# Kernel tuning notes

Measured on AMD Instinct MI355X. Metric: run time of the kernel, lower is better.

Reference implementation:

```python
import jax, jax.numpy as jnp
import numpy as np

K_BITS = 4
V_BITS = 4
GROUP_SIZE = 64
EPS = 1e-8


def _quant_dequant_per_token(x, bits):
    # TurboQuantProd: symmetric per-token (per head_dim vector) absmax quantization.
    qmax = 2.0 ** (bits - 1) - 1.0
    scale = jnp.maximum(jnp.max(jnp.abs(x), axis=-1, keepdims=True) / qmax, EPS)
    return jnp.clip(jnp.round(x / scale), -qmax, qmax) * scale


def _quant_dequant_grouped(x, bits, group_size):
    # TurboQuantValue: symmetric grouped absmax quantization along head_dim.
    shp = x.shape
    xg = x.reshape(shp[:-1] + (shp[-1] // group_size, group_size))
    qmax = 2.0 ** (bits - 1) - 1.0
    scale = jnp.maximum(jnp.max(jnp.abs(xg), axis=-1, keepdims=True) / qmax, EPS)
    dq = jnp.clip(jnp.round(xg / scale), -qmax, qmax) * scale
    return dq.reshape(shp)


def setup_inputs() -> dict:
    key = jax.random.key(0)
    kq, kk, kv = jax.random.split(key, 3)
    B, H, S, D = 2, 16, 2048, 128
    query = jax.random.normal(kq, (B, H, S, D), dtype=jnp.float32)
    k = jax.random.normal(kk, (B, H, S, D), dtype=jnp.float32)
    v = jax.random.normal(kv, (B, H, S, D), dtype=jnp.float32)
    causal_mask = jnp.tril(jnp.ones((S, S), dtype=bool))[None, None]  # [1,1,S,S]
    return {"query": query, "key": k, "value": v, "causal_mask": causal_mask}


def reference(query, key, value, causal_mask):
    # Non-protected path: quantize K per-token, V grouped, then fused dequant + SDPA.
    head_dim = query.shape[-1]
    scale = 1.0 / np.sqrt(head_dim).astype(np.float32)
    dq_key = _quant_dequant_per_token(key, K_BITS)
    dq_value = _quant_dequant_grouped(value, V_BITS, GROUP_SIZE)
    scores = jnp.einsum('bhqd,bhkd->bhqk', query, dq_key) * scale
    scores = jnp.where(causal_mask, scores, -jnp.inf)
    weights = jax.nn.softmax(scores, axis=-1)
    output = jnp.einsum('bhqk,bhkd->bhqd', weights, dq_value)
    return (output, weights)
```

## Files before the change

### kernel.cpp

```cpp
#include <hip/hip_runtime.h>

#define SQ 2048
#define DD 128
#define BHN 32
#define SC2 0.12751741934f

typedef __attribute__((ext_vector_type(8))) short bf16x8;
typedef __attribute__((ext_vector_type(4))) float f32x4;

__device__ __forceinline__ unsigned short f2bf(float x){
  unsigned int u = __float_as_uint(x);
  unsigned int r = (u + 0x7FFFu + ((u >> 16) & 1u)) >> 16;
  return (unsigned short)r;
}
__device__ __forceinline__ unsigned pack2bf(float a, float b){
  return (unsigned)f2bf(a) | ((unsigned)f2bf(b) << 16);
}

__device__ __forceinline__ void gl_lds16(const void* g, void* l){
  __builtin_amdgcn_global_load_lds(
      (const __attribute__((address_space(1))) unsigned int*)g,
      (__attribute__((address_space(3))) unsigned int*)l, 16, 0, 0);
}

__device__ __forceinline__ void nt_store4(float* p, f32x4 v){
  __builtin_nontemporal_store(v, (f32x4*)p);
}

__global__ __launch_bounds__(256) void qd_kernel(const float* __restrict__ K,
                                                 const float* __restrict__ V,
                                                 char* __restrict__ dqK,
                                                 char* __restrict__ dqVt){
  __shared__ float Vlds[128*65];
  const int t = threadIdx.x;
  const int bh = blockIdx.x >> 5;
  const int stile = blockIdx.x & 31;
  const int tt = t >> 2;
  const int q4 = t & 3;
  const int s = stile*64 + tt;
  const long ebase = ((long)(bh*SQ + s))*DD + 32*q4;

  float vals[32];
  {
    const float4* kp = (const float4*)(K + ebase);
    float am = 0.f;
    #pragma unroll
    for (int j=0;j<8;j++){
      float4 v4 = kp[j];
      vals[4*j+0]=v4.x; vals[4*j+1]=v4.y; vals[4*j+2]=v4.z; vals[4*j+3]=v4.w;
      am = fmaxf(am, fmaxf(fmaxf(fabsf(v4.x),fabsf(v4.y)),fmaxf(fabsf(v4.z),fabsf(v4.w))));
    }
    am = fmaxf(am, __shfl_xor(am,1));
    am = fmaxf(am, __shfl_xor(am,2));
    const float sc = fmaxf(am/7.0f, 1e-8f);
    #pragma unroll
    for (int j=0;j<32;j++){
      float qv = rintf(vals[j]/sc);
      qv = fminf(7.f, fmaxf(-7.f, qv));
      vals[j] = qv*sc;
    }
    const long rowb = ((long)(bh*SQ + s))*256;
    const int swz = (s & 7) << 4;
    #pragma unroll
    for (int c=0;c<4;c++){
      uint4 w;
      w.x = pack2bf(vals[8*c+0], vals[8*c+1]);
      w.y = pack2bf(vals[8*c+2], vals[8*c+3]);
      w.z = pack2bf(vals[8*c+4], vals[8*c+5]);
      w.w = pack2bf(vals[8*c+6], vals[8*c+7]);
      *(uint4*)(dqK + rowb + ((64*q4 + 16*c) ^ swz)) = w;
    }
  }
  {
    const float4* vp = (const float4*)(V + ebase);
    float am = 0.f;
    #pragma unroll
    for (int j=0;j<8;j++){
      float4 v4 = vp[j];
      vals[4*j+0]=v4.x; vals[4*j+1]=v4.y; vals[4*j+2]=v4.z; vals[4*j+3]=v4.w;
      am = fmaxf(am, fmaxf(fmaxf(fabsf(v4.x),fabsf(v4.y)),fmaxf(fabsf(v4.z),fabsf(v4.w))));
    }
    am = fmaxf(am, __shfl_xor(am,1));
    const float sc = fmaxf(am/7.0f, 1e-8f);
    #pragma unroll
    for (int j=0;j<32;j++){
      float qv = rintf(vals[j]/sc);
      qv = fminf(7.f, fmaxf(-7.f, qv));
      Vlds[(32*q4 + j)*65 + tt] = qv*sc;
    }
  }
  __syncthreads();
  #pragma unroll
  for (int m=0;m<4;m++){
    const int chunk = m*256 + t;
    const int d = chunk >> 3;
    const int c = chunk & 7;
    uint4 w;
    const float* f = &Vlds[d*65 + 8*c];
    w.x = pack2bf(f[0], f[1]);
    w.y = pack2bf(f[2], f[3]);
    w.z = pack2bf(f[4], f[5]);
    w.w = pack2bf(f[6], f[7]);
    const long ob = ((long)(bh*DD + d))*4096 + (long)stile*128 + ((16*c) ^ ((d&7)<<4));
    *(uint4*)(dqVt + ob) = w;
  }
}

__global__ __launch_bounds__(256,2) void attn_fused(const float* __restrict__ Q,
    const char* __restrict__ dqK, const char* __restrict__ dqVt,
    float* __restrict__ Out, float* __restrict__ Wout){
  __shared__ __attribute__((aligned(16))) char Kt[2][16384];
  __shared__ __attribute__((aligned(16))) char Vt[2][16384];
  __shared__ __attribute__((aligned(16))) char Et[4][4096];

  const int bid = blockIdx.x;
  const int xcd = bid & 7;
  const int loc = bid >> 3;
  const int bh  = xcd*4 + (loc & 3);
  const int p   = loc >> 2;
  const int t = threadIdx.x;
  const int lane = t & 63;
  const int w = t >> 6;
  const int s = w >> 1;
  const int ws = w & 1;
  const int l15 = lane & 15, l4 = lane >> 4;
  const int swz = (l15 & 7) << 4;

  const int qt   = s ? p : (31 - p);
  const int q0   = qt * 64;
  const int nktA = 32 - p;
  const int myNkt = qt + 1;
  const int rbase = q0 + 32*ws;

  bf16x8 qa[2][4];
  #pragma unroll
  for (int g=0; g<2; ++g){
    const float* qb = Q + ((long)(bh*SQ) + rbase + 16*g + l15)*DD + 8*l4;
    #pragma unroll
    for (int kk=0;kk<4;kk++){
      float4 a = *(const float4*)(qb + 32*kk);
      float4 b = *(const float4*)(qb + 32*kk + 4);
      bf16x8 r;
      r[0]=(short)f2bf(a.x); r[1]=(short)f2bf(a.y); r[2]=(short)f2bf(a.z); r[3]=(short)f2bf(a.w);
      r[4]=(short)f2bf(b.x); r[5]=(short)f2bf(b.y); r[6]=(short)f2bf(b.z); r[7]=(short)f2bf(b.w);
      qa[g][kk]=r;
    }
  }

  const char* Kb = dqK + (long)bh*SQ*256;
  const char* Vb = dqVt + (long)bh*DD*4096;

  const f32x4 z4 = {0.f,0.f,0.f,0.f};
  f32x4 oacc[2][8] = {{z4,z4,z4,z4,z4,z4,z4,z4},{z4,z4,z4,z4,z4,z4,z4,z4}};
  float ssum[2] = {0.f, 0.f};
  char* eb = &Et[w][0];

  auto stageKV = [&](int buf, int kt){
    const char* ks = Kb + (long)kt*16384;
    #pragma unroll
    for (int i=0;i<4;i++)
      gl_lds16(ks + i*4096 + t*16, &Kt[buf][i*4096 + t*16]);
    const char* vs = Vb + (long)kt*128;
    #pragma unroll
    for (int i=0;i<4;i++)
      gl_lds16(vs + (long)(i*32 + (t>>3))*4096 + (t&7)*16, &Vt[buf][i*4096 + t*16]);
  };

  stageKV(0, 0);
  __syncthreads();
  int cur = 0;
  for (int kt=0; kt<nktA; ++kt){
    if (kt+1 < nktA) stageKV(cur^1, kt+1);

    if (kt < myNkt){
      f32x4 sacc[2][4] = {{z4,z4,z4,z4},{z4,z4,z4,z4}};
      {
        const char* kbase = &Kt[cur][0] + l15*256;
        __builtin_amdgcn_s_setprio(1);
        #pragma unroll
        for (int cf=0;cf<4;cf++){
          #pragma unroll
          for (int kk=0;kk<4;kk++){
            bf16x8 kb = *(const bf16x8*)(kbase + cf*4096 + ((64*kk+16*l4) ^ swz));
            sacc[0][cf] = __builtin_amdgcn_mfma_f32_16x16x32_bf16(kb, qa[0][kk], sacc[0][cf], 0,0,0);
            sacc[1][cf] = __builtin_amdgcn_mfma_f32_16x16x32_bf16(kb, qa[1][kk], sacc[1][cf], 0,0,0);
          }
        }
        __builtin_amdgcn_s_setprio(0);
      }

      const int k0 = kt*64;
      if (kt < qt){
        #pragma unroll
        for (int g=0; g<2; ++g){
          const int lr = 16*g + l15;
          #pragma unroll
          for (int cf=0;cf<4;cf++){
            float e0 = exp2f(sacc[g][cf][0]*SC2);
            float e1 = exp2f(sacc[g][cf][1]*SC2);
            float e2 = exp2f(sacc[g][cf][2]*SC2);
            float e3 = exp2f(sacc[g][cf][3]*SC2);
            ssum[g] += (e0+e1) + (e2+e3);
            uint2 wp; wp.x = pack2bf(e0,e1); wp.y = pack2bf(e2,e3);
            *(uint2*)(eb + lr*128 + ((32*cf + 8*l4) ^ swz)) = wp;
          }
        }
      } else {
        #pragma unroll
        for (int g=0; g<2; ++g){
          const int lr = 16*g + l15;
          const int qrow = rbase + lr;
          #pragma unroll
          for (int cf=0;cf<4;cf++){
            const int tok0 = k0 + 16*cf + 4*l4;
            float e0 = (tok0+0 <= qrow) ? exp2f(sacc[g][cf][0]*SC2) : 0.f;
            float e1 = (tok0+1 <= qrow) ? exp2f(sacc[g][cf][1]*SC2) : 0.f;
            float e2 = (tok0+2 <= qrow) ? exp2f(sacc[g][cf][2]*SC2) : 0.f;
            float e3 = (tok0+3 <= qrow) ? exp2f(sacc[g][cf][3]*SC2) : 0.f;
            ssum[g] += (e0+e1) + (e2+e3);
            uint2 wp; wp.x = pack2bf(e0,e1); wp.y = pack2bf(e2,e3);
            *(uint2*)(eb + lr*128 + ((32*cf + 8*l4) ^ swz)) = wp;
          }
        }
      }

      {
        const char* vbase = &Vt[cur][0] + l15*128;
        __builtin_amdgcn_s_setprio(1);
        #pragma unroll
        for (int kc=0;kc<2;kc++){
          const int eo = (64*kc + 16*l4) ^ swz;
          bf16x8 ea0 = *(const bf16x8*)(eb + l15*128 + eo);
          bf16x8 ea1 = *(const bf16x8*)(eb + (16+l15)*128 + eo);
          #pragma unroll
          for (int df=0;df<8;df++){
            bf16x8 vv = *(const bf16x8*)(vbase + df*2048 + eo);
            oacc[0][df] = __builtin_amdgcn_mfma_f32_16x16x32_bf16(ea0, vv, oacc[0][df], 0,0,0);
            oacc[1][df] = __builtin_amdgcn_mfma_f32_16x16x32_bf16(ea1, vv, oacc[1][df], 0,0,0);
          }
        }
        __builtin_amdgcn_s_setprio(0);
      }
    }
    __syncthreads();
    cur ^= 1;
  }

  float si[2];
  #pragma unroll
  for (int g=0; g<2; ++g){
    float sm = ssum[g];
    sm += __shfl_xor(sm, 16);
    sm += __shfl_xor(sm, 32);
    si[g] = 1.0f / sm;
    float invr[4];
    #pragma unroll
    for (int i=0;i<4;i++) invr[i] = __shfl(si[g], 4*l4+i);
    float* ob = Out + ((long)(bh*SQ) + rbase + 16*g)*DD;
    #pragma unroll
    for (int df=0;df<8;df++){
      #pragma unroll
      for (int i=0;i<4;i++)
        ob[(4*l4+i)*DD + 16*df + l15] = oacc[g][df][i]*invr[i];
    }
  }

  float* Wbase = Wout + (long)bh*SQ*SQ;
  float* wrow0 = Wbase + (long)(rbase + l15)*SQ;
  float* wrow1 = Wbase + (long)(rbase + 16 + l15)*SQ;

  for (int kt=0; kt<myNkt; ++kt){
    const int k0 = kt*64;
    const char* kr = Kb + (long)kt*16384 + l15*256;

    bf16x8 kb[4][4];
    #pragma unroll
    for (int cf=0;cf<4;cf++){
      #pragma unroll
      for (int kk=0;kk<4;kk++)
        kb[cf][kk] = *(const bf16x8*)(kr + cf*4096 + ((64*kk+16*l4) ^ swz));
    }

    f32x4 sacc[2][4] = {{z4,z4,z4,z4},{z4,z4,z4,z4}};
    __builtin_amdgcn_s_setprio(1);
    #pragma unroll
    for (int cf=0;cf<4;cf++){
      #pragma unroll
      for (int kk=0;kk<4;kk++){
        sacc[0][cf] = __builtin_amdgcn_mfma_f32_16x16x32_bf16(kb[cf][kk], qa[0][kk], sacc[0][cf], 0,0,0);
        sacc[1][cf] = __builtin_amdgcn_mfma_f32_16x16x32_bf16(kb[cf][kk], qa[1][kk], sacc[1][cf], 0,0,0);
      }
    }
    __builtin_amdgcn_s_setprio(0);

    if (kt < qt){
      #pragma unroll
      for (int cf=0;cf<4;cf++){
        const int tok0 = k0 + 16*cf + 4*l4;
        f32x4 wv;
        wv[0] = exp2f(sacc[0][cf][0]*SC2)*si[0];
        wv[1] = exp2f(sacc[0][cf][1]*SC2)*si[0];
        wv[2] = exp2f(sacc[0][cf][2]*SC2)*si[0];
        wv[3] = exp2f(sacc[0][cf][3]*SC2)*si[0];
        nt_store4(wrow0 + tok0, wv);
        wv[0] = exp2f(sacc[1][cf][0]*SC2)*si[1];
        wv[1] = exp2f(sacc[1][cf][1]*SC2)*si[1];
        wv[2] = exp2f(sacc[1][cf][2]*SC2)*si[1];
        wv[3] = exp2f(sacc[1][cf][3]*SC2)*si[1];
        nt_store4(wrow1 + tok0, wv);
      }
    } else {
      const int qrow0 = rbase + l15;
      const int qrow1 = rbase + 16 + l15;
      #pragma unroll
      for (int cf=0;cf<4;cf++){
        const int tok0 = k0 + 16*cf + 4*l4;
        f32x4 wv;
        wv[0] = (tok0+0 <= qrow0) ? exp2f(sacc[0][cf][0]*SC2)*si[0] : 0.f;
        wv[1] = (tok0+1 <= qrow0) ? exp2f(sacc[0][cf][1]*SC2)*si[0] : 0.f;
        wv[2] = (tok0+2 <= qrow0) ? exp2f(sacc[0][cf][2]*SC2)*si[0] : 0.f;
        wv[3] = (tok0+3 <= qrow0) ? exp2f(sacc[0][cf][3]*SC2)*si[0] : 0.f;
        nt_store4(wrow0 + tok0, wv);
        wv[0] = (tok0+0 <= qrow1) ? exp2f(sacc[1][cf][0]*SC2)*si[1] : 0.f;
        wv[1] = (tok0+1 <= qrow1) ? exp2f(sacc[1][cf][1]*SC2)*si[1] : 0.f;
        wv[2] = (tok0+2 <= qrow1) ? exp2f(sacc[1][cf][2]*SC2)*si[1] : 0.f;
        wv[3] = (tok0+3 <= qrow1) ? exp2f(sacc[1][cf][3]*SC2)*si[1] : 0.f;
        nt_store4(wrow1 + tok0, wv);
      }
    }
  }

  const int z0 = myNkt*64;
  if (z0 < SQ){
    const f32x4 zz = {0.f,0.f,0.f,0.f};
    for (int rr=0;rr<32;rr++){
      float* row = Wbase + (long)(rbase + rr)*SQ;
      for (int c = z0 + 4*lane; c < SQ; c += 256)
        nt_store4(row + c, zz);
    }
  }
}

extern "C" void kernel_launch(void* const* d_in, const int* in_sizes, int n_in,
                              void* d_out, int out_size, void* d_ws, size_t ws_size,
                              hipStream_t stream) {
  const float* Q = (const float*)d_in[0];
  const float* K = (const float*)d_in[1];
  const float* V = (const float*)d_in[2];
  float* Out = (float*)d_out;
  float* Wout = (float*)d_out + (size_t)BHN*SQ*DD;
  char* dqK  = (char*)d_ws;
  char* dqVt = (char*)d_ws + (size_t)BHN*SQ*DD*2;

  qd_kernel<<<BHN*32, 256, 0, stream>>>(K, V, dqK, dqVt);
  attn_fused<<<512, 256, 0, stream>>>(Q, dqK, dqVt, Out, Wout);
}
```

Measured before the change: 261.9 us.

## Pair long and short query tiles per wave and use plain stores for weights

Each wave now owns 16 rows of a long tile (qtA = 31-p) and 16 rows of a short tile (qtB = p), instead of splitting waves into long and short halves. Every wave therefore does about the same work, and the B half of the MFMA work is skipped once it passes its causal limit. Block ordering also changes so that p interleaves small and large values. The weight and zero-fill stores switch from nontemporal to ordinary stores. The aim is to remove intra-block wave imbalance, since short-tile waves used to sit idle at barriers; the cost is extra branching inside the loops.

```diff
diff --git a/kernel.cpp b/kernel.cpp
--- a/kernel.cpp
+++ b/kernel.cpp
@@ -21,10 +21,6 @@
   __builtin_amdgcn_global_load_lds(
       (const __attribute__((address_space(1))) unsigned int*)g,
       (__attribute__((address_space(3))) unsigned int*)l, 16, 0, 0);
-}
-
-__device__ __forceinline__ void nt_store4(float* p, f32x4 v){
-  __builtin_nontemporal_store(v, (f32x4*)p);
 }
 
 __global__ __launch_bounds__(256) void qd_kernel(const float* __restrict__ K,
@@ -117,25 +113,26 @@
   const int xcd = bid & 7;
   const int loc = bid >> 3;
   const int bh  = xcd*4 + (loc & 3);
-  const int p   = loc >> 2;
+  const int i   = loc >> 2;
+  const int p   = (i < 8) ? i : (23 - i);
   const int t = threadIdx.x;
   const int lane = t & 63;
   const int w = t >> 6;
-  const int s = w >> 1;
-  const int ws = w & 1;
   const int l15 = lane & 15, l4 = lane >> 4;
   const int swz = (l15 & 7) << 4;
 
-  const int qt   = s ? p : (31 - p);
-  const int q0   = qt * 64;
-  const int nktA = 32 - p;
-  const int myNkt = qt + 1;
-  const int rbase = q0 + 32*ws;
+  const int qtA = 31 - p, qtB = p;
+  const int q0A = qtA*64, q0B = qtB*64;
+  const int nktA = qtA + 1;
+  const int nktB = qtB + 1;
+  const int rA = q0A + 16*w + l15;
+  const int rB = q0B + 16*w + l15;
 
   bf16x8 qa[2][4];
   #pragma unroll
   for (int g=0; g<2; ++g){
-    const float* qb = Q + ((long)(bh*SQ) + rbase + 16*g + l15)*DD + 8*l4;
+    const int qrow = g ? rB : rA;
+    const float* qb = Q + ((long)(bh*SQ) + qrow)*DD + 8*l4;
     #pragma unroll
     for (int kk=0;kk<4;kk++){
       float4 a = *(const float4*)(qb + 32*kk);
@@ -158,12 +155,12 @@
   auto stageKV = [&](int buf, int kt){
     const char* ks = Kb + (long)kt*16384;
     #pragma unroll
-    for (int i=0;i<4;i++)
-      gl_lds16(ks + i*4096 + t*16, &Kt[buf][i*4096 + t*16]);
+    for (int it=0;it<4;it++)
+      gl_lds16(ks + it*4096 + t*16, &Kt[buf][it*4096 + t*16]);
     const char* vs = Vb + (long)kt*128;
     #pragma unroll
-    for (int i=0;i<4;i++)
-      gl_lds16(vs + (long)(i*32 + (t>>3))*4096 + (t&7)*16, &Vt[buf][i*4096 + t*16]);
+    for (int it=0;it<4;it++)
+      gl_lds16(vs + (long)(it*32 + (t>>3))*4096 + (t&7)*16, &Vt[buf][it*4096 + t*16]);
   };
 
   stageKV(0, 0);
@@ -171,12 +168,14 @@
   int cur = 0;
   for (int kt=0; kt<nktA; ++kt){
     if (kt+1 < nktA) stageKV(cur^1, kt+1);
-
-    if (kt < myNkt){
-      f32x4 sacc[2][4] = {{z4,z4,z4,z4},{z4,z4,z4,z4}};
-      {
-        const char* kbase = &Kt[cur][0] + l15*256;
-        __builtin_amdgcn_s_setprio(1);
+    const bool doB = (kt < nktB);
+    const int k0 = kt*64;
+
+    f32x4 sacc[2][4] = {{z4,z4,z4,z4},{z4,z4,z4,z4}};
+    {
+      const char* kbase = &Kt[cur][0] + l15*256;
+      __builtin_amdgcn_s_setprio(1);
+      if (doB){
         #pragma unroll
         for (int cf=0;cf<4;cf++){
           #pragma unroll
@@ -186,47 +185,77 @@
             sacc[1][cf] = __builtin_amdgcn_mfma_f32_16x16x32_bf16(kb, qa[1][kk], sacc[1][cf], 0,0,0);
           }
         }
-        __builtin_amdgcn_s_setprio(0);
-      }
-
-      const int k0 = kt*64;
-      if (kt < qt){
-        #pragma unroll
-        for (int g=0; g<2; ++g){
-          const int lr = 16*g + l15;
+      } else {
+        #pragma unroll
+        for (int cf=0;cf<4;cf++){
           #pragma unroll
-          for (int cf=0;cf<4;cf++){
-            float e0 = exp2f(sacc[g][cf][0]*SC2);
-            float e1 = exp2f(sacc[g][cf][1]*SC2);
-            float e2 = exp2f(sacc[g][cf][2]*SC2);
-            float e3 = exp2f(sacc[g][cf][3]*SC2);
-            ssum[g] += (e0+e1) + (e2+e3);
-            uint2 wp; wp.x = pack2bf(e0,e1); wp.y = pack2bf(e2,e3);
-            *(uint2*)(eb + lr*128 + ((32*cf + 8*l4) ^ swz)) = wp;
+          for (int kk=0;kk<4;kk++){
+            bf16x8 kb = *(const bf16x8*)(kbase + cf*4096 + ((64*kk+16*l4) ^ swz));
+            sacc[0][cf] = __builtin_amdgcn_mfma_f32_16x16x32_bf16(kb, qa[0][kk], sacc[0][cf], 0,0,0);
           }
         }
+      }
+      __builtin_amdgcn_s_setprio(0);
+    }
+
+    {
+      if (kt < qtA){
+        #pragma unroll
+        for (int cf=0;cf<4;cf++){
+          float e0 = exp2f(sacc[0][cf][0]*SC2);
+          float e1 = exp2f(sacc[0][cf][1]*SC2);
+          float e2 = exp2f(sacc[0][cf][2]*SC2);
+          float e3 = exp2f(sacc[0][cf][3]*SC2);
+          ssum[0] += (e0+e1) + (e2+e3);
+          uint2 wp; wp.x = pack2bf(e0,e1); wp.y = pack2bf(e2,e3);
+          *(uint2*)(eb + l15*128 + ((32*cf + 8*l4) ^ swz)) = wp;
+        }
       } else {
         #pragma unroll
-        for (int g=0; g<2; ++g){
-          const int lr = 16*g + l15;
-          const int qrow = rbase + lr;
-          #pragma unroll
-          for (int cf=0;cf<4;cf++){
-            const int tok0 = k0 + 16*cf + 4*l4;
-            float e0 = (tok0+0 <= qrow) ? exp2f(sacc[g][cf][0]*SC2) : 0.f;
-            float e1 = (tok0+1 <= qrow) ? exp2f(sacc[g][cf][1]*SC2) : 0.f;
-            float e2 = (tok0+2 <= qrow) ? exp2f(sacc[g][cf][2]*SC2) : 0.f;
-            float e3 = (tok0+3 <= qrow) ? exp2f(sacc[g][cf][3]*SC2) : 0.f;
-            ssum[g] += (e0+e1) + (e2+e3);
-            uint2 wp; wp.x = pack2bf(e0,e1); wp.y = pack2bf(e2,e3);
-            *(uint2*)(eb + lr*128 + ((32*cf + 8*l4) ^ swz)) = wp;
-          }
-        }
-      }
-
-      {
-        const char* vbase = &Vt[cur][0] + l15*128;
-        __builtin_amdgcn_s_setprio(1);
+        for (int cf=0;cf<4;cf++){
+          const int tok0 = k0 + 16*cf + 4*l4;
+          float e0 = (tok0+0 <= rA) ? exp2f(sacc[0][cf][0]*SC2) : 0.f;
+          float e1 = (tok0+1 <= rA) ? exp2f(sacc[0][cf][1]*SC2) : 0.f;
+          float e2 = (tok0+2 <= rA) ? exp2f(sacc[0][cf][2]*SC2) : 0.f;
+          float e3 = (tok0+3 <= rA) ? exp2f(sacc[0][cf][3]*SC2) : 0.f;
+          ssum[0] += (e0+e1) + (e2+e3);
+          uint2 wp; wp.x = pack2bf(e0,e1); wp.y = pack2bf(e2,e3);
+          *(uint2*)(eb + l15*128 + ((32*cf + 8*l4) ^ swz)) = wp;
+        }
+      }
+    }
+    if (doB){
+      const int lr = 16 + l15;
+      if (kt < qtB){
+        #pragma unroll
+        for (int cf=0;cf<4;cf++){
+          float e0 = exp2f(sacc[1][cf][0]*SC2);
+          float e1 = exp2f(sacc[1][cf][1]*SC2);
+          float e2 = exp2f(sacc[1][cf][2]*SC2);
+          float e3 = exp2f(sacc[1][cf][3]*SC2);
+          ssum[1] += (e0+e1) + (e2+e3);
+          uint2 wp; wp.x = pack2bf(e0,e1); wp.y = pack2bf(e2,e3);
+          *(uint2*)(eb + lr*128 + ((32*cf + 8*l4) ^ swz)) = wp;
+        }
+      } else {
+        #pragma unroll
+        for (int cf=0;cf<4;cf++){
+          const int tok0 = k0 + 16*cf + 4*l4;
+          float e0 = (tok0+0 <= rB) ? exp2f(sacc[1][cf][0]*SC2) : 0.f;
+          float e1 = (tok0+1 <= rB) ? exp2f(sacc[1][cf][1]*SC2) : 0.f;
+          float e2 = (tok0+2 <= rB) ? exp2f(sacc[1][cf][2]*SC2) : 0.f;
+          float e3 = (tok0+3 <= rB) ? exp2f(sacc[1][cf][3]*SC2) : 0.f;
+          ssum[1] += (e0+e1) + (e2+e3);
+          uint2 wp; wp.x = pack2bf(e0,e1); wp.y = pack2bf(e2,e3);
+          *(uint2*)(eb + lr*128 + ((32*cf + 8*l4) ^ swz)) = wp;
+        }
+      }
+    }
+
+    {
+      const char* vbase = &Vt[cur][0] + l15*128;
+      __builtin_amdgcn_s_setprio(1);
+      if (doB){
         #pragma unroll
         for (int kc=0;kc<2;kc++){
           const int eo = (64*kc + 16*l4) ^ swz;
@@ -239,8 +268,19 @@
             oacc[1][df] = __builtin_amdgcn_mfma_f32_16x16x32_bf16(ea1, vv, oacc[1][df], 0,0,0);
           }
         }
-        __builtin_amdgcn_s_setprio(0);
-      }
+      } else {
+        #pragma unroll
+        for (int kc=0;kc<2;kc++){
+          const int eo = (64*kc + 16*l4) ^ swz;
+          bf16x8 ea0 = *(const bf16x8*)(eb + l15*128 + eo);
+          #pragma unroll
+          for (int df=0;df<8;df++){
+            bf16x8 vv = *(const bf16x8*)(vbase + df*2048 + eo);
+            oacc[0][df] = __builtin_amdgcn_mfma_f32_16x16x32_bf16(ea0, vv, oacc[0][df], 0,0,0);
+          }
+        }
+      }
+      __builtin_amdgcn_s_setprio(0);
     }
     __syncthreads();
     cur ^= 1;
@@ -255,23 +295,25 @@
     si[g] = 1.0f / sm;
     float invr[4];
     #pragma unroll
-    for (int i=0;i<4;i++) invr[i] = __shfl(si[g], 4*l4+i);
-    float* ob = Out + ((long)(bh*SQ) + rbase + 16*g)*DD;
+    for (int ii=0;ii<4;ii++) invr[ii] = __shfl(si[g], 4*l4+ii);
+    const int rb0 = (g ? q0B : q0A) + 16*w;
+    float* ob = Out + ((long)(bh*SQ) + rb0)*DD;
     #pragma unroll
     for (int df=0;df<8;df++){
       #pragma unroll
-      for (int i=0;i<4;i++)
-        ob[(4*l4+i)*DD + 16*df + l15] = oacc[g][df][i]*invr[i];
+      for (int ii=0;ii<4;ii++)
+        ob[(4*l4+ii)*DD + 16*df + l15] = oacc[g][df][ii]*invr[ii];
     }
   }
 
   float* Wbase = Wout + (long)bh*SQ*SQ;
-  float* wrow0 = Wbase + (long)(rbase + l15)*SQ;
-  float* wrow1 = Wbase + (long)(rbase + 16 + l15)*SQ;
-
-  for (int kt=0; kt<myNkt; ++kt){
+  float* wrowA = Wbase + (long)rA*SQ;
+  float* wrowB = Wbase + (long)rB*SQ;
+
+  for (int kt=0; kt<nktA; ++kt){
     const int k0 = kt*64;
     const char* kr = Kb + (long)kt*16384 + l15*256;
+    const bool doB = (kt < nktB);
 
     bf16x8 kb[4][4];
     #pragma unroll
@@ -283,17 +325,26 @@
 
     f32x4 sacc[2][4] = {{z4,z4,z4,z4},{z4,z4,z4,z4}};
     __builtin_amdgcn_s_setprio(1);
-    #pragma unroll
-    for (int cf=0;cf<4;cf++){
-      #pragma unroll
-      for (int kk=0;kk<4;kk++){
-        sacc[0][cf] = __builtin_amdgcn_mfma_f32_16x16x32_bf16(kb[cf][kk], qa[0][kk], sacc[0][cf], 0,0,0);
-        sacc[1][cf] = __builtin_amdgcn_mfma_f32_16x16x32_bf16(kb[cf][kk], qa[1][kk], sacc[1][cf], 0,0,0);
+    if (doB){
+      #pragma unroll
+      for (int cf=0;cf<4;cf++){
+        #pragma unroll
+        for (int kk=0;kk<4;kk++){
+          sacc[0][cf] = __builtin_amdgcn_mfma_f32_16x16x32_bf16(kb[cf][kk], qa[0][kk], sacc[0][cf], 0,0,0);
+          sacc[1][cf] = __builtin_amdgcn_mfma_f32_16x16x32_bf16(kb[cf][kk], qa[1][kk], sacc[1][cf], 0,0,0);
+        }
+      }
+    } else {
+      #pragma unroll
+      for (int cf=0;cf<4;cf++){
+        #pragma unroll
+        for (int kk=0;kk<4;kk++)
+          sacc[0][cf] = __builtin_amdgcn_mfma_f32_16x16x32_bf16(kb[cf][kk], qa[0][kk], sacc[0][cf], 0,0,0);
       }
     }
     __builtin_amdgcn_s_setprio(0);
 
-    if (kt < qt){
+    if (kt < qtA){
       #pragma unroll
       for (int cf=0;cf<4;cf++){
         const int tok0 = k0 + 16*cf + 4*l4;
@@ -302,41 +353,62 @@
         wv[1] = exp2f(sacc[0][cf][1]*SC2)*si[0];
         wv[2] = exp2f(sacc[0][cf][2]*SC2)*si[0];
         wv[3] = exp2f(sacc[0][cf][3]*SC2)*si[0];
-        nt_store4(wrow0 + tok0, wv);
-        wv[0] = exp2f(sacc[1][cf][0]*SC2)*si[1];
-        wv[1] = exp2f(sacc[1][cf][1]*SC2)*si[1];
-        wv[2] = exp2f(sacc[1][cf][2]*SC2)*si[1];
-        wv[3] = exp2f(sacc[1][cf][3]*SC2)*si[1];
-        nt_store4(wrow1 + tok0, wv);
+        *(f32x4*)(wrowA + tok0) = wv;
       }
     } else {
-      const int qrow0 = rbase + l15;
-      const int qrow1 = rbase + 16 + l15;
       #pragma unroll
       for (int cf=0;cf<4;cf++){
         const int tok0 = k0 + 16*cf + 4*l4;
         f32x4 wv;
-        wv[0] = (tok0+0 <= qrow0) ? exp2f(sacc[0][cf][0]*SC2)*si[0] : 0.f;
-        wv[1] = (tok0+1 <= qrow0) ? exp2f(sacc[0][cf][1]*SC2)*si[0] : 0.f;
-        wv[2] = (tok0+2 <= qrow0) ? exp2f(sacc[0][cf][2]*SC2)*si[0] : 0.f;
-        wv[3] = (tok0+3 <= qrow0) ? exp2f(sacc[0][cf][3]*SC2)*si[0] : 0.f;
-        nt_store4(wrow0 + tok0, wv);
-        wv[0] = (tok0+0 <= qrow1) ? exp2f(sacc[1][cf][0]*SC2)*si[1] : 0.f;
-        wv[1] = (tok0+1 <= qrow1) ? exp2f(sacc[1][cf][1]*SC2)*si[1] : 0.f;
-        wv[2] = (tok0+2 <= qrow1) ? exp2f(sacc[1][cf][2]*SC2)*si[1] : 0.f;
-        wv[3] = (tok0+3 <= qrow1) ? exp2f(sacc[1][cf][3]*SC2)*si[1] : 0.f;
-        nt_store4(wrow1 + tok0, wv);
-      }
-    }
-  }
-
-  const int z0 = myNkt*64;
-  if (z0 < SQ){
-    const f32x4 zz = {0.f,0.f,0.f,0.f};
-    for (int rr=0;rr<32;rr++){
-      float* row = Wbase + (long)(rbase + rr)*SQ;
+        wv[0] = (tok0+0 <= rA) ? exp2f(sacc[0][cf][0]*SC2)*si[0] : 0.f;
+        wv[1] = (tok0+1 <= rA) ? exp2f(sacc[0][cf][1]*SC2)*si[0] : 0.f;
+        wv[2] = (tok0+2 <= rA) ? exp2f(sacc[0][cf][2]*SC2)*si[0] : 0.f;
+        wv[3] = (tok0+3 <= rA) ? exp2f(sacc[0][cf][3]*SC2)*si[0] : 0.f;
+        *(f32x4*)(wrowA + tok0) = wv;
+      }
+    }
+    if (doB){
+      if (kt < qtB){
+        #pragma unroll
+        for (int cf=0;cf<4;cf++){
+          const int tok0 = k0 + 16*cf + 4*l4;
+          f32x4 wv;
+          wv[0] = exp2f(sacc[1][cf][0]*SC2)*si[1];
+          wv[1] = exp2f(sacc[1][cf][1]*SC2)*si[1];
+          wv[2] = exp2f(sacc[1][cf][2]*SC2)*si[1];
+          wv[3] = exp2f(sacc[1][cf][3]*SC2)*si[1];
+          *(f32x4*)(wrowB + tok0) = wv;
+        }
+      } else {
+        #pragma unroll
+        for (int cf=0;cf<4;cf++){
+          const int tok0 = k0 + 16*cf + 4*l4;
+          f32x4 wv;
+          wv[0] = (tok0+0 <= rB) ? exp2f(sacc[1][cf][0]*SC2)*si[1] : 0.f;
+          wv[1] = (tok0+1 <= rB) ? exp2f(sacc[1][cf][1]*SC2)*si[1] : 0.f;
+          wv[2] = (tok0+2 <= rB) ? exp2f(sacc[1][cf][2]*SC2)*si[1] : 0.f;
+          wv[3] = (tok0+3 <= rB) ? exp2f(sacc[1][cf][3]*SC2)*si[1] : 0.f;
+          *(f32x4*)(wrowB + tok0) = wv;
+        }
+      }
+    }
+  }
+
+  const f32x4 zz = {0.f,0.f,0.f,0.f};
+  {
+    const int z0 = nktA*64;
+    for (int rr=0; rr<16 && z0 < SQ; rr++){
+      float* row = Wbase + (long)(q0A + 16*w + rr)*SQ;
       for (int c = z0 + 4*lane; c < SQ; c += 256)
-        nt_store4(row + c, zz);
+        *(f32x4*)(row + c) = zz;
+    }
+  }
+  {
+    const int z0 = nktB*64;
+    for (int rr=0; rr<16; rr++){
+      float* row = Wbase + (long)(q0B + 16*w + rr)*SQ;
+      for (int c = z0 + 4*lane; c < SQ; c += 256)
+        *(f32x4*)(row + c) = zz;
     }
   }
 }
```

Result: faster. 232.7 us (-11.1%).
